# Performance work log

Hardware: AMD Instinct MI355X
Metric: run time of the kernel (lower is better)

Reference implementation:

```python
import jax, jax.numpy as jnp
import numpy as np

B, T, DIN = 4, 1024, 512
DLIN, DK, DV, NH = 1024, 1024, 1024, 16

def setup_inputs() -> dict:
    key = jax.random.key(0)
    ks = jax.random.split(key, 5)
    s = 0.02
    return {
        "data": jax.random.normal(ks[0], (B, T, DIN), dtype=jnp.float32),
        "W_in": jax.random.normal(ks[1], (DLIN, DIN + T), dtype=jnp.float32) * s,
        "W_q": jax.random.normal(ks[2], (DK, DLIN), dtype=jnp.float32) * s,
        "W_k": jax.random.normal(ks[3], (DK, DLIN), dtype=jnp.float32) * s,
        "W_v": jax.random.normal(ks[4], (DV, DLIN), dtype=jnp.float32) * s,
    }

def reference(data, W_in, W_q, W_k, W_v):
    b, t, d_in = data.shape
    nh = NH
    dk = DK // nh
    dv = DV // nh
    scale = 1.0 / np.sqrt(dk).astype(np.float32)
    # concat identity positional one-hots: [B, T, DIN + T]
    p = jnp.broadcast_to(jnp.eye(t, dtype=data.dtype), (b, t, t))
    x = jnp.concatenate([data, p], axis=-1)
    h = jnp.einsum('btc,dc->btd', x, W_in)            # [B,T,DLIN]
    q = jnp.einsum('btd,kd->btk', h, W_q).reshape(b, t, nh, dk).transpose(0, 2, 1, 3)
    k = jnp.einsum('btd,kd->btk', h, W_k).reshape(b, t, nh, dk).transpose(0, 2, 1, 3)
    v = jnp.einsum('btd,kd->btk', h, W_v).reshape(b, t, nh, dv).transpose(0, 2, 1, 3)
    dist = jnp.einsum('bhqd,bhkd->bhqk', q, k) * scale   # [B,H,T,T]
    dist = jax.nn.softmax(dist, axis=-1)
    att = jnp.einsum('bhqk,bhkd->bhqd', dist, v)         # [B,H,T,dv]
    return att.transpose(0, 2, 1, 3).reshape(b, t, DV)
```

## Files before the change

kernel.cpp:

```cpp
#include <hip/hip_runtime.h>
#include <stdint.h>


typedef __bf16 bf16x8 __attribute__((ext_vector_type(8)));
typedef __bf16 bf16x4v __attribute__((ext_vector_type(4)));
typedef float f32x4 __attribute__((ext_vector_type(4)));
typedef float f32x16 __attribute__((ext_vector_type(16)));
typedef unsigned short u16;
typedef u16 u16x8 __attribute__((ext_vector_type(8)));

#define MFMA16(a, b, c) __builtin_amdgcn_mfma_f32_16x16x32_bf16(a, b, c, 0, 0, 0)
#define MFMA32(a, b, c) __builtin_amdgcn_mfma_f32_32x32x16_bf16(a, b, c, 0, 0, 0)

using gld_src_t = const __attribute__((address_space(1))) unsigned int*;
using gld_dst_t = __attribute__((address_space(3))) unsigned int*;

__device__ __forceinline__ u16 f2bf(float f) {
  uint32_t u = __builtin_bit_cast(uint32_t, f);
  uint32_t r = (u + 0x7fffu + ((u >> 16) & 1u)) >> 16;
  return (u16)r;
}


__global__ __launch_bounds__(256) void cvt_all(
    const float* __restrict__ data, const float* __restrict__ wq,
    const float* __restrict__ wk, const float* __restrict__ wv,
    u16* __restrict__ o_data, u16* __restrict__ o_wq,
    u16* __restrict__ o_wk, u16* __restrict__ o_wv) {
  const float* s;
  u16* o;
  int n;
  switch (blockIdx.y) {
    case 0: s = data; o = o_data; n = 4096 * 512; break;
    case 1: s = wq; o = o_wq; n = 1024 * 1024; break;
    case 2: s = wk; o = o_wk; n = 1024 * 1024; break;
    default: s = wv; o = o_wv; n = 1024 * 1024; break;
  }
  int i = (blockIdx.x * 256 + threadIdx.x) * 8;
  if (i >= n) return;
  float4 a = *(const float4*)(s + i);
  float4 b = *(const float4*)(s + i + 4);
  u16x8 v;
  v[0] = f2bf(a.x); v[1] = f2bf(a.y); v[2] = f2bf(a.z); v[3] = f2bf(a.w);
  v[4] = f2bf(b.x); v[5] = f2bf(b.y); v[6] = f2bf(b.z); v[7] = f2bf(b.w);
  *(u16x8*)(o + i) = v;
}

__global__ __launch_bounds__(256) void cvt_win(const float* __restrict__ Win,
                                               u16* __restrict__ wd) {
  int i = (blockIdx.x * 256 + threadIdx.x) * 8;
  if (i >= 1024 * 512) return;
  int row = i >> 9, col = i & 511;
  const float* s = Win + (size_t)row * 1536 + col;
  float4 a = *(const float4*)s;
  float4 b = *(const float4*)(s + 4);
  u16x8 v;
  v[0] = f2bf(a.x); v[1] = f2bf(a.y); v[2] = f2bf(a.z); v[3] = f2bf(a.w);
  v[4] = f2bf(b.x); v[5] = f2bf(b.y); v[6] = f2bf(b.z); v[7] = f2bf(b.w);
  *(u16x8*)(wd + i) = v;
}


template <int EPI>
__global__ __launch_bounds__(256) void gemm_bt(
    const u16* __restrict__ A, const u16* __restrict__ B0,
    const u16* __restrict__ B1, const u16* __restrict__ B2,
    const float* __restrict__ Wpos, u16* __restrict__ O0,
    u16* __restrict__ O1, u16* __restrict__ O2, int K) {
  __shared__ u16 Ash[128 * 64];
  __shared__ u16 Bsh[128 * 64];
  const int tid = threadIdx.x;
  const int lane = tid & 63;
  const int w = tid >> 6;
  const int wr = w >> 1, wc = w & 1;
  const int m0 = blockIdx.x * 128, n0 = blockIdx.y * 128;

  const u16* Bw;
  u16* Out;
  if constexpr (EPI == 0) {
    Bw = B0; Out = O0;
  } else {
    int z = blockIdx.z;
    Bw = (z == 0) ? B0 : (z == 1) ? B1 : B2;
    Out = (z == 0) ? O0 : (z == 1) ? O1 : O2;
  }

  f32x4 acc[4][4];
#pragma unroll
  for (int m = 0; m < 4; ++m)
#pragma unroll
    for (int n = 0; n < 4; ++n) acc[m][n] = (f32x4){0.f, 0.f, 0.f, 0.f};

  for (int kt = 0; kt < K; kt += 64) {
    __syncthreads();
#pragma unroll
    for (int i = 0; i < 4; ++i) {
      int c = i * 256 + tid;
      int row = c >> 3;
      int sg = (c & 7) ^ (row & 7);
      const u16* srcA = A + (size_t)(m0 + row) * K + kt + sg * 8;
      __builtin_amdgcn_global_load_lds((gld_src_t)srcA,
                                       (gld_dst_t)&Ash[(i * 256 + w * 64) * 8],
                                       16, 0, 0);
      const u16* srcB = Bw + (size_t)(n0 + row) * K + kt + sg * 8;
      __builtin_amdgcn_global_load_lds((gld_src_t)srcB,
                                       (gld_dst_t)&Bsh[(i * 256 + w * 64) * 8],
                                       16, 0, 0);
    }
    __syncthreads();
#pragma unroll
    for (int kk = 0; kk < 2; ++kk) {
      bf16x8 af[4], bfr[4];
#pragma unroll
      for (int m = 0; m < 4; ++m) {
        int r = wr * 64 + m * 16 + (lane & 15);
        int slot = (kk * 4 + (lane >> 4)) ^ (r & 7);
        af[m] = *(const bf16x8*)((const char*)Ash + r * 128 + slot * 16);
      }
#pragma unroll
      for (int n = 0; n < 4; ++n) {
        int r = wc * 64 + n * 16 + (lane & 15);
        int slot = (kk * 4 + (lane >> 4)) ^ (r & 7);
        bfr[n] = *(const bf16x8*)((const char*)Bsh + r * 128 + slot * 16);
      }
#pragma unroll
      for (int m = 0; m < 4; ++m)
#pragma unroll
        for (int n = 0; n < 4; ++n) acc[m][n] = MFMA16(af[m], bfr[n], acc[m][n]);
    }
  }

#pragma unroll
  for (int m = 0; m < 4; ++m) {
#pragma unroll
    for (int n = 0; n < 4; ++n) {
      int r0 = m0 + wr * 64 + m * 16 + ((lane >> 4) << 2);
      int col = n0 + wc * 64 + n * 16 + (lane & 15);
      if constexpr (EPI == 0) {
        int t0 = r0 & 1023;
        float4 pb = *(const float4*)(Wpos + (size_t)col * 1536 + 512 + t0);
        float pbv[4] = {pb.x, pb.y, pb.z, pb.w};
#pragma unroll
        for (int q = 0; q < 4; ++q)
          Out[(size_t)(r0 + q) * 1024 + col] = f2bf(acc[m][n][q] + pbv[q]);
      } else {
        float qsc = (blockIdx.z == 0) ? 0.18033688011112042f : 1.0f;
        int hd = col >> 6, j = col & 63;
        int b = r0 >> 10;
        size_t bh = (size_t)(b * 16 + hd) * 65536;
#pragma unroll
        for (int q = 0; q < 4; ++q) {
          int t = (r0 + q) & 1023;
          size_t idx = (blockIdx.z == 2) ? bh + (size_t)j * 1024 + t
                                         : bh + (size_t)t * 64 + j;
          Out[idx] = f2bf(acc[m][n][q] * qsc);
        }
      }
    }
  }
}

__global__ __launch_bounds__(256, 2) void attn(const u16* __restrict__ Q,
                                               const u16* __restrict__ K,
                                               const u16* __restrict__ Vt,
                                               float* __restrict__ out) {
  __shared__ float lbuf[4][32 * 66];
  const int tid = threadIdx.x, lane = tid & 63, w = tid >> 6;
  const int q = lane & 31, hi = lane >> 5;
  const int flat = blockIdx.x;
  const int bh = (flat & 7) * 8 + ((flat >> 3) & 7);
  const int q0 = (flat >> 6) * 128 + w * 32;
  const size_t base = (size_t)bh * 65536;

  bf16x8 qf[4];
#pragma unroll
  for (int ks = 0; ks < 4; ++ks)
    qf[ks] = *(const bf16x8*)(Q + base + (size_t)(q0 + q) * 64 + ks * 16 + hi * 8);

  f32x16 ot[2];
#pragma unroll
  for (int r = 0; r < 16; ++r) {
    ot[0][r] = 0.f;
    ot[1][r] = 0.f;
  }
  float lsum = 0.f;

  const u16* Kp = K + base + (size_t)q * 64 + hi * 8;
  const u16* Vp = Vt + base + (size_t)q * 1024 + hi * 4;

  for (int kv0 = 0; kv0 < 1024; kv0 += 32) {
    f32x16 st;
#pragma unroll
    for (int r = 0; r < 16; ++r) st[r] = 0.f;
#pragma unroll
    for (int ks = 0; ks < 4; ++ks) {
      bf16x8 kf = *(const bf16x8*)(Kp + (size_t)kv0 * 64 + ks * 16);
      st = MFMA32(kf, qf[ks], st);
    }
    float pe[16];
#pragma unroll
    for (int r = 0; r < 16; ++r) pe[r] = __builtin_exp2f(st[r]);
    {
      float t0 = (pe[0] + pe[1]) + (pe[2] + pe[3]);
      float t1 = (pe[4] + pe[5]) + (pe[6] + pe[7]);
      float t2 = (pe[8] + pe[9]) + (pe[10] + pe[11]);
      float t3 = (pe[12] + pe[13]) + (pe[14] + pe[15]);
      lsum += (t0 + t1) + (t2 + t3);
    }
#pragma unroll
    for (int s = 0; s < 2; ++s) {
      bf16x8 pf;
#pragma unroll
      for (int j = 0; j < 8; ++j) pf[j] = (__bf16)pe[8 * s + j];
#pragma unroll
      for (int d = 0; d < 2; ++d) {
        const u16* vr = Vp + (size_t)(32 * d) * 1024 + kv0 + 16 * s;
        bf16x4v v0 = *(const bf16x4v*)vr;
        bf16x4v v1 = *(const bf16x4v*)(vr + 8);
        bf16x8 vf;
#pragma unroll
        for (int j = 0; j < 4; ++j) {
          vf[j] = v0[j];
          vf[4 + j] = v1[j];
        }
        ot[d] = MFMA32(vf, pf, ot[d]);
      }
    }
  }

  lsum += __shfl_xor(lsum, 32, 64);
  float ri = 1.0f / lsum;

  float* lb = &lbuf[w][0];
#pragma unroll
  for (int d = 0; d < 2; ++d)
#pragma unroll
    for (int rr = 0; rr < 16; rr += 2) {
      int dv = 32 * d + (rr & 3) + 8 * (rr >> 2) + 4 * hi;
      *(float2*)(lb + q * 66 + dv) =
          make_float2(ot[d][rr] * ri, ot[d][rr + 1] * ri);
    }
  __syncthreads();
  const int b = bh >> 4, hd = bh & 15;
#pragma unroll
  for (int i = 0; i < 8; ++i) {
    int row = i * 4 + (lane >> 4);
    const float* lr = lb + row * 66 + (lane & 15) * 4;
    float2 x0 = *(const float2*)lr;
    float2 x1 = *(const float2*)(lr + 2);
    float4 v = make_float4(x0.x, x0.y, x1.x, x1.y);
    *(float4*)(out + ((size_t)(b * 1024 + q0 + row)) * 1024 + hd * 64 +
               (lane & 15) * 4) = v;
  }
}


extern "C" void kernel_launch(void* const* d_in, const int* in_sizes, int n_in,
                              void* d_out, int out_size, void* d_ws,
                              size_t ws_size, hipStream_t stream) {
  const float* data = (const float*)d_in[0];
  const float* Win = (const float*)d_in[1];
  const float* Wq = (const float*)d_in[2];
  const float* Wk = (const float*)d_in[3];
  const float* Wv = (const float*)d_in[4];
  float* out = (float*)d_out;

  char* ws = (char*)d_ws;
  u16* data_b = (u16*)ws; ws += (size_t)4096 * 512 * 2;
  u16* wd_b = (u16*)ws;   ws += (size_t)1024 * 512 * 2;
  u16* wq_b = (u16*)ws;   ws += (size_t)1024 * 1024 * 2;
  u16* wk_b = (u16*)ws;   ws += (size_t)1024 * 1024 * 2;
  u16* wv_b = (u16*)ws;   ws += (size_t)1024 * 1024 * 2;
  u16* h_b = (u16*)ws;    ws += (size_t)4096 * 1024 * 2;
  u16* q_b = (u16*)ws;    ws += (size_t)4194304 * 2;
  u16* k_b = (u16*)ws;    ws += (size_t)4194304 * 2;
  u16* vt_b = (u16*)ws;   ws += (size_t)4194304 * 2;

  cvt_all<<<dim3(1024, 4), 256, 0, stream>>>(data, Wq, Wk, Wv, data_b, wq_b,
                                             wk_b, wv_b);
  cvt_win<<<dim3(256), 256, 0, stream>>>(Win, wd_b);
  gemm_bt<0><<<dim3(32, 8, 1), 256, 0, stream>>>(data_b, wd_b, wd_b, wd_b, Win,
                                                 h_b, h_b, h_b, 512);
  gemm_bt<1><<<dim3(32, 8, 3), 256, 0, stream>>>(h_b, wq_b, wk_b, wv_b, nullptr,
                                                 q_b, k_b, vt_b, 1024);
  attn<<<dim3(512), 256, 0, stream>>>(q_b, k_b, vt_b, out);
}
```

Baseline: 217.0 us.

## Permute Vt layout for 16-byte loads and double-buffer K/V in attention loop

The projection epilogue now writes V-transposed with key indices bits 2 and 3 swapped. Each lane's 8 bf16 values for the PV MFMA then sit contiguously and load as one 16-byte vector instead of two 8-byte loads plus shuffles. The attention loop is also restructured into a two-stage register double buffer, so the next tile's K and V loads are issued before the current tile is computed, hiding global load latency. The cost is extra VGPRs for the second buffer, which could reduce occupancy under the launch bounds of 256 threads with 2 blocks.

```diff
diff --git a/kernel.cpp b/kernel.cpp
--- a/kernel.cpp
+++ b/kernel.cpp
@@ -3,7 +3,6 @@
 
 
 typedef __bf16 bf16x8 __attribute__((ext_vector_type(8)));
-typedef __bf16 bf16x4v __attribute__((ext_vector_type(4)));
 typedef float f32x4 __attribute__((ext_vector_type(4)));
 typedef float f32x16 __attribute__((ext_vector_type(16)));
 typedef unsigned short u16;
@@ -151,7 +150,8 @@
 #pragma unroll
         for (int q = 0; q < 4; ++q) {
           int t = (r0 + q) & 1023;
-          size_t idx = (blockIdx.z == 2) ? bh + (size_t)j * 1024 + t
+          int tp = (t & ~12) | ((t & 4) << 1) | ((t & 8) >> 1);
+          size_t idx = (blockIdx.z == 2) ? bh + (size_t)j * 1024 + tp
                                          : bh + (size_t)t * 64 + j;
           Out[idx] = f2bf(acc[m][n][q] * qsc);
         }
@@ -186,17 +186,27 @@
   float lsum = 0.f;
 
   const u16* Kp = K + base + (size_t)q * 64 + hi * 8;
-  const u16* Vp = Vt + base + (size_t)q * 1024 + hi * 4;
-
-  for (int kv0 = 0; kv0 < 1024; kv0 += 32) {
+  const u16* Vp = Vt + base + (size_t)q * 1024 + hi * 8;
+
+  auto loadK = [&](int kv0, bf16x8 (&kb)[4]) {
+#pragma unroll
+    for (int ks = 0; ks < 4; ++ks)
+      kb[ks] = *(const bf16x8*)(Kp + (size_t)kv0 * 64 + ks * 16);
+  };
+  auto loadV = [&](int kv0, bf16x8 (&vb)[4]) {
+#pragma unroll
+    for (int s = 0; s < 2; ++s)
+#pragma unroll
+      for (int d = 0; d < 2; ++d)
+        vb[2 * s + d] =
+            *(const bf16x8*)(Vp + (size_t)(32 * d) * 1024 + kv0 + 16 * s);
+  };
+  auto compute = [&](const bf16x8 (&kb)[4], const bf16x8 (&vb)[4]) {
     f32x16 st;
 #pragma unroll
     for (int r = 0; r < 16; ++r) st[r] = 0.f;
 #pragma unroll
-    for (int ks = 0; ks < 4; ++ks) {
-      bf16x8 kf = *(const bf16x8*)(Kp + (size_t)kv0 * 64 + ks * 16);
-      st = MFMA32(kf, qf[ks], st);
-    }
+    for (int ks = 0; ks < 4; ++ks) st = MFMA32(kb[ks], qf[ks], st);
     float pe[16];
 #pragma unroll
     for (int r = 0; r < 16; ++r) pe[r] = __builtin_exp2f(st[r]);
@@ -213,19 +223,22 @@
 #pragma unroll
       for (int j = 0; j < 8; ++j) pf[j] = (__bf16)pe[8 * s + j];
 #pragma unroll
-      for (int d = 0; d < 2; ++d) {
-        const u16* vr = Vp + (size_t)(32 * d) * 1024 + kv0 + 16 * s;
-        bf16x4v v0 = *(const bf16x4v*)vr;
-        bf16x4v v1 = *(const bf16x4v*)(vr + 8);
-        bf16x8 vf;
-#pragma unroll
-        for (int j = 0; j < 4; ++j) {
-          vf[j] = v0[j];
-          vf[4 + j] = v1[j];
-        }
-        ot[d] = MFMA32(vf, pf, ot[d]);
-      }
-    }
+      for (int d = 0; d < 2; ++d) ot[d] = MFMA32(vb[2 * s + d], pf, ot[d]);
+    }
+  };
+
+  bf16x8 kA[4], vA[4], kB[4], vB[4];
+  loadK(0, kA);
+  loadV(0, vA);
+  for (int kv0 = 0; kv0 < 1024; kv0 += 64) {
+    loadK(kv0 + 32, kB);
+    loadV(kv0 + 32, vB);
+    compute(kA, vA);
+    if (kv0 + 64 < 1024) {
+      loadK(kv0 + 64, kA);
+      loadV(kv0 + 64, vA);
+    }
+    compute(kB, vB);
   }
 
   lsum += __shfl_xor(lsum, 32, 64);
```

Measured after the change: 193.6 us. 1.12x faster.

## Stage K/V tiles through double-buffered LDS shared across waves in attention

Applied to the files above, without the earlier changes.

The attention kernel now has the whole block cooperatively load 64-key K and V tiles into double-buffered LDS, prefetching the next tile into registers while the current one is computed. Before, each wave read K and V straight from global memory with redundant per-wave loads. The Vt layout written by the QKV projection epilogue is permuted along the token dimension so each lane reads V fragments as single contiguous 16-byte vectors instead of two 8-byte pieces. This adds a block-wide barrier per tile and more shared memory, which may reduce occupancy.

```diff
diff --git a/kernel.cpp b/kernel.cpp
--- a/kernel.cpp
+++ b/kernel.cpp
@@ -3,7 +3,6 @@
 
 
 typedef __bf16 bf16x8 __attribute__((ext_vector_type(8)));
-typedef __bf16 bf16x4v __attribute__((ext_vector_type(4)));
 typedef float f32x4 __attribute__((ext_vector_type(4)));
 typedef float f32x16 __attribute__((ext_vector_type(16)));
 typedef unsigned short u16;
@@ -151,7 +150,8 @@
 #pragma unroll
         for (int q = 0; q < 4; ++q) {
           int t = (r0 + q) & 1023;
-          size_t idx = (blockIdx.z == 2) ? bh + (size_t)j * 1024 + t
+          int tp = (t & ~12) | ((t & 4) << 1) | ((t & 8) >> 1);
+          size_t idx = (blockIdx.z == 2) ? bh + (size_t)j * 1024 + tp
                                          : bh + (size_t)t * 64 + j;
           Out[idx] = f2bf(acc[m][n][q] * qsc);
         }
@@ -164,7 +164,9 @@
                                                const u16* __restrict__ K,
                                                const u16* __restrict__ Vt,
                                                float* __restrict__ out) {
-  __shared__ float lbuf[4][32 * 66];
+  __shared__ __align__(16) u16 smem[2 * 64 * 68 * 2];
+  u16* const Klds = smem;
+  u16* const Vlds = smem + 2 * 64 * 68;
   const int tid = threadIdx.x, lane = tid & 63, w = tid >> 6;
   const int q = lane & 31, hi = lane >> 5;
   const int flat = blockIdx.x;
@@ -177,68 +179,101 @@
   for (int ks = 0; ks < 4; ++ks)
     qf[ks] = *(const bf16x8*)(Q + base + (size_t)(q0 + q) * 64 + ks * 16 + hi * 8);
 
-  f32x16 ot[2];
+  f32x16 od[2];
 #pragma unroll
   for (int r = 0; r < 16; ++r) {
-    ot[0][r] = 0.f;
-    ot[1][r] = 0.f;
+    od[0][r] = 0.f;
+    od[1][r] = 0.f;
   }
   float lsum = 0.f;
 
-  const u16* Kp = K + base + (size_t)q * 64 + hi * 8;
-  const u16* Vp = Vt + base + (size_t)q * 1024 + hi * 4;
-
-  for (int kv0 = 0; kv0 < 1024; kv0 += 32) {
-    f32x16 st;
-#pragma unroll
-    for (int r = 0; r < 16; ++r) st[r] = 0.f;
-#pragma unroll
-    for (int ks = 0; ks < 4; ++ks) {
-      bf16x8 kf = *(const bf16x8*)(Kp + (size_t)kv0 * 64 + ks * 16);
-      st = MFMA32(kf, qf[ks], st);
-    }
-    float pe[16];
-#pragma unroll
-    for (int r = 0; r < 16; ++r) pe[r] = __builtin_exp2f(st[r]);
-    {
-      float t0 = (pe[0] + pe[1]) + (pe[2] + pe[3]);
-      float t1 = (pe[4] + pe[5]) + (pe[6] + pe[7]);
-      float t2 = (pe[8] + pe[9]) + (pe[10] + pe[11]);
-      float t3 = (pe[12] + pe[13]) + (pe[14] + pe[15]);
-      lsum += (t0 + t1) + (t2 + t3);
-    }
-#pragma unroll
-    for (int s = 0; s < 2; ++s) {
-      bf16x8 pf;
-#pragma unroll
-      for (int j = 0; j < 8; ++j) pf[j] = (__bf16)pe[8 * s + j];
-#pragma unroll
-      for (int d = 0; d < 2; ++d) {
-        const u16* vr = Vp + (size_t)(32 * d) * 1024 + kv0 + 16 * s;
-        bf16x4v v0 = *(const bf16x4v*)vr;
-        bf16x4v v1 = *(const bf16x4v*)(vr + 8);
-        bf16x8 vf;
-#pragma unroll
-        for (int j = 0; j < 4; ++j) {
-          vf[j] = v0[j];
-          vf[4 + j] = v1[j];
+  const u16* Kg = K + base;
+  const u16* Vg = Vt + base;
+  const int srow = tid >> 3, sch = tid & 7;
+
+  bf16x8 kst[2], vst[2];
+  auto gload = [&](int kv0) {
+    kst[0] = *(const bf16x8*)(Kg + (size_t)(kv0 + srow) * 64 + sch * 8);
+    kst[1] = *(const bf16x8*)(Kg + (size_t)(kv0 + srow + 32) * 64 + sch * 8);
+    vst[0] = *(const bf16x8*)(Vg + (size_t)srow * 1024 + kv0 + sch * 8);
+    vst[1] = *(const bf16x8*)(Vg + (size_t)(srow + 32) * 1024 + kv0 + sch * 8);
+  };
+  auto swrite = [&](int buf) {
+    u16* kd = Klds + buf * (64 * 68);
+    u16* vd = Vlds + buf * (64 * 68);
+    *(bf16x8*)(kd + srow * 68 + sch * 8) = kst[0];
+    *(bf16x8*)(kd + (srow + 32) * 68 + sch * 8) = kst[1];
+    *(bf16x8*)(vd + srow * 68 + sch * 8) = vst[0];
+    *(bf16x8*)(vd + (srow + 32) * 68 + sch * 8) = vst[1];
+  };
+  auto compute = [&](int buf) {
+    const u16* kb = Klds + buf * (64 * 68);
+    const u16* vb = Vlds + buf * (64 * 68);
+#pragma unroll
+    for (int u = 0; u < 2; ++u) {
+      f32x16 st;
+#pragma unroll
+      for (int r = 0; r < 16; ++r) st[r] = 0.f;
+#pragma unroll
+      for (int ks = 0; ks < 4; ++ks) {
+        bf16x8 kf =
+            *(const bf16x8*)(kb + (u * 32 + q) * 68 + ks * 16 + hi * 8);
+        st = MFMA32(kf, qf[ks], st);
+      }
+      float pe[16];
+#pragma unroll
+      for (int r = 0; r < 16; ++r) pe[r] = __builtin_exp2f(st[r]);
+      {
+        float t0 = (pe[0] + pe[1]) + (pe[2] + pe[3]);
+        float t1 = (pe[4] + pe[5]) + (pe[6] + pe[7]);
+        float t2 = (pe[8] + pe[9]) + (pe[10] + pe[11]);
+        float t3 = (pe[12] + pe[13]) + (pe[14] + pe[15]);
+        lsum += (t0 + t1) + (t2 + t3);
+      }
+#pragma unroll
+      for (int s = 0; s < 2; ++s) {
+        bf16x8 pf;
+#pragma unroll
+        for (int j = 0; j < 8; ++j) pf[j] = (__bf16)pe[8 * s + j];
+#pragma unroll
+        for (int d = 0; d < 2; ++d) {
+          bf16x8 vf = *(const bf16x8*)(vb + (q + 32 * d) * 68 + u * 32 +
+                                       s * 16 + hi * 8);
+          od[d] = MFMA32(vf, pf, od[d]);
         }
-        ot[d] = MFMA32(vf, pf, ot[d]);
-      }
+      }
+    }
+  };
+
+  gload(0);
+  swrite(0);
+  __syncthreads();
+  int buf = 0;
+  for (int t = 0; t < 16; ++t) {
+    if (t < 15) {
+      gload((t + 1) * 64);
+      __builtin_amdgcn_sched_barrier(0);
+    }
+    compute(buf);
+    if (t < 15) {
+      swrite(buf ^ 1);
+      __syncthreads();
+      buf ^= 1;
     }
   }
 
   lsum += __shfl_xor(lsum, 32, 64);
   float ri = 1.0f / lsum;
 
-  float* lb = &lbuf[w][0];
+  __syncthreads();
+  float* lb = (float*)smem + w * (32 * 66);
 #pragma unroll
   for (int d = 0; d < 2; ++d)
 #pragma unroll
     for (int rr = 0; rr < 16; rr += 2) {
       int dv = 32 * d + (rr & 3) + 8 * (rr >> 2) + 4 * hi;
       *(float2*)(lb + q * 66 + dv) =
-          make_float2(ot[d][rr] * ri, ot[d][rr + 1] * ri);
+          make_float2(od[d][rr] * ri, od[d][rr + 1] * ri);
     }
   __syncthreads();
   const int b = bh >> 4, hd = bh & 15;
```

Measured after the change: 200.4 us. 7.7% less time.
